# Performance work log

Measured on AMD Instinct MI355X. Metric: run time of the kernel, lower is better.

The kernel has to match this reference:

```python
import jax, jax.numpy as jnp
import numpy as np

B, L, C = 2, 8192, 256
K, NLEV = 17, 4
HALF = K // 2


def setup_inputs() -> dict:
    key = jax.random.key(0)
    ks = jax.random.split(key, 10)
    s = 0.02
    return {
        "x": jax.random.normal(ks[0], (B, L, C), jnp.float32),
        "stem_w": jax.random.normal(ks[1], (C, C, 2), jnp.float32) * s,   # Conv1d (out,in,k)
        "stem_b": jax.random.normal(ks[2], (C,), jnp.float32) * s,
        "qkv_w": jax.random.normal(ks[3], (3 * C, C), jnp.float32) * s,
        "width_w": jax.random.normal(ks[4], (1, C), jnp.float32) * s,
        "width_b": jax.random.normal(ks[5], (1,), jnp.float32) * s,
        "out_w": jax.random.normal(ks[6], (C, C), jnp.float32) * s,
        "query": jax.random.normal(ks[7], (NLEV * C,), jnp.float32) * s,
        "film_w": jax.random.normal(ks[8], (2 * C, NLEV * C), jnp.float32) * s,
        "film_b": jax.random.normal(ks[9], (2 * C,), jnp.float32) * s,
    }


def _local_attn(h, qkv_w, width_w, width_b, out_w):
    # h: (b, l, c); 1D local windowed attention with learned sigmoid distance mask
    b, l, c = h.shape
    rel_dist = jnp.abs(jnp.arange(K, dtype=h.dtype) - HALF)  # (K,)
    max_dist = float(HALF)
    scale = c ** -0.5
    qkv = h @ qkv_w.T
    q, k, v = jnp.split(qkv, 3, axis=-1)
    width = jax.nn.sigmoid(h @ width_w.T + width_b) * max_dist + 0.5  # (b,l,1)
    k_pad = jnp.pad(k, ((0, 0), (HALF, HALF), (0, 0)))
    v_pad = jnp.pad(v, ((0, 0), (HALF, HALF), (0, 0)))
    idx = jnp.arange(l)[:, None] + jnp.arange(K)[None, :]  # (l,K) indices into padded seq
    k_win = k_pad[:, idx]  # (b,l,K,c)
    v_win = v_pad[:, idx]  # (b,l,K,c)
    scores = jnp.einsum('blc,blwc->blw', q, k_win) * scale
    soft_mask = jax.nn.sigmoid((width - rel_dist) * 5.0)  # (b,l,K)
    scores = scores - (1.0 - soft_mask) * 10000.0
    attn = jax.nn.softmax(scores, axis=-1)
    o = jnp.einsum('blw,blwc->blc', attn, v_win)
    return (o + v) @ out_w.T


def _forward(x, stem_w, stem_b, qkv_w, width_w, width_b, out_w, query, film_w, film_b):
    b, l, c = x.shape
    # stem conv: Conv1d(C, C, kernel=2, padding=1), then narrow to first l positions
    h = jnp.transpose(x, (0, 2, 1))  # (B,C,L)
    h = jax.lax.conv_general_dilated(h, stem_w, (1,), [(1, 1)],
                                     dimension_numbers=('NCH', 'OIH', 'NCH'))
    h = h[:, :, :l] + stem_b[None, :, None]
    h = jnp.transpose(h, (0, 2, 1))  # (B,L,C)
    levels = []
    for i in range(NLEV):
        h = _local_attn(h, qkv_w, width_w, width_b, out_w)
        levels.append(h)
        if i < NLEV - 1:  # avg_pool(kernel=2, stride=2)
            bl = h.shape[1]
            h = h.reshape(b, bl // 2, 2, c).mean(axis=2)
    # nearest upsample each coarser level back to L (factors are exact powers of 2)
    ups = [levels[0]]
    for lvl in levels[1:]:
        ups.append(jnp.repeat(lvl, l // lvl.shape[1], axis=1))
    concat = jnp.concatenate(ups, axis=-1)  # (B,L,NLEV*C)
    gattn = jax.nn.softmax(concat @ query, axis=-1)  # (B,L)
    global_ctx = jnp.einsum('bl,bld->bd', gattn, concat)  # (B,NLEV*C)
    film = global_ctx @ film_w.T + film_b  # (B,2C)
    scale_f, bias_f = jnp.split(film, 2, axis=-1)
    return levels[0] * (1.0 + scale_f[:, None, :]) + bias_f[:, None, :]


def reference(x, stem_w, stem_b, qkv_w, width_w, width_b, out_w, query, film_w, film_b):
    return _forward(x, stem_w, stem_b, qkv_w, width_w, width_b, out_w, query, film_w, film_b)
```

## Files before the change

### kernel.cpp

```cpp
#include <hip/hip_runtime.h>
#include <math.h>

#define L_SEQ 8192
#define B_SZ  2
#define CH    256
#define NLEV  4

typedef __attribute__((ext_vector_type(8))) short bf16x8;
typedef __attribute__((ext_vector_type(4))) float f32x4;

static __device__ __forceinline__ float sigmoidf_(float x) {
    return 1.0f / (1.0f + expf(-x));
}

static __device__ __forceinline__ float bf2f_(unsigned short u) {
    union { unsigned int ui; float f; } x;
    x.ui = ((unsigned int)u) << 16;
    return x.f;
}
static __device__ __forceinline__ unsigned short f2b_(float f) {
    union { float f; unsigned int u; } x;
    x.f = f;
    unsigned int lsb = (x.u >> 16) & 1u;
    unsigned int r = x.u + 0x7fffu + lsb;
    return (unsigned short)(r >> 16);
}
static __device__ __forceinline__ float4 ldb4_(const unsigned short* p) {
    ushort4 u = *(const ushort4*)p;
    return make_float4(bf2f_(u.x), bf2f_(u.y), bf2f_(u.z), bf2f_(u.w));
}

__global__ void prep_kernel(const float* __restrict__ x,
                            const float* __restrict__ qkv_w,
                            const float* __restrict__ out_w,
                            const float* __restrict__ stem_w,
                            unsigned short* __restrict__ x16g,
                            unsigned short* __restrict__ qw16,
                            unsigned short* __restrict__ ow16,
                            unsigned short* __restrict__ sw16)
{
    int i = blockIdx.x * 256 + threadIdx.x;
    if (i < 256) { x16g[i] = 0; return; }
    i -= 256;
    if (i < 4194304) { x16g[256 + i] = f2b_(x[i]); return; }
    i -= 4194304;
    if (i < 196608) { qw16[i] = f2b_(qkv_w[i]); return; }
    i -= 196608;
    if (i < 65536) { ow16[i] = f2b_(out_w[i]); return; }
    i -= 65536;
    {
        int k = i & 511, n = i >> 9;
        float v = (k < 256) ? stem_w[(size_t)n * 512 + k * 2]
                            : stem_w[(size_t)n * 512 + (k - 256) * 2 + 1];
        sw16[i] = f2b_(v);
    }
}

__global__ __launch_bounds__(256) void stem_gemm_bf16(
    const unsigned short* __restrict__ x16g, const unsigned short* __restrict__ W,
    unsigned short* __restrict__ outB, const float* __restrict__ bias)
{
    __shared__ unsigned short As[128 * 32];
    __shared__ unsigned short Bs[128 * 32];
    const int tid  = threadIdx.x;
    const int wave = tid >> 6;
    const int lane = tid & 63;
    const int bm = blockIdx.y * 128;
    const int bn = blockIdx.x * 128;
    const int wm = (wave & 1) * 64;
    const int wn = (wave >> 1) * 64;
    const int srow = lane >> 2;
    const int scol = (lane & 3) * 8;

    f32x4 acc[4][4] = {};

    for (int k0 = 0; k0 < 512; k0 += 32) {
        __syncthreads();
        #pragma unroll
        for (int c = 0; c < 2; ++c) {
            const int chunk = c * 4 + wave;
            const int row = bm + chunk * 16 + srow;
            const int t = row & (L_SEQ - 1);
            const unsigned short* ga;
            if (k0 < 256)
                ga = x16g + (t > 0 ? (size_t)row * 256 : 0) + k0 + scol;
            else
                ga = x16g + ((size_t)row + 1) * 256 + (k0 - 256) + scol;
            const unsigned short* gw = W + (size_t)(bn + chunk * 16 + srow) * 512 + k0 + scol;
            __builtin_amdgcn_global_load_lds(
                (const __attribute__((address_space(1))) void*)ga,
                (__attribute__((address_space(3))) void*)(As + chunk * 16 * 32),
                16, 0, 0);
            __builtin_amdgcn_global_load_lds(
                (const __attribute__((address_space(1))) void*)gw,
                (__attribute__((address_space(3))) void*)(Bs + chunk * 16 * 32),
                16, 0, 0);
        }
        __syncthreads();

        bf16x8 af[4], bf[4];
        const int fr = lane & 15;
        const int kk = (lane >> 4) * 8;
        #pragma unroll
        for (int i = 0; i < 4; ++i) {
            af[i] = *(const bf16x8*)(As + (wm + i * 16 + fr) * 32 + kk);
            bf[i] = *(const bf16x8*)(Bs + (wn + i * 16 + fr) * 32 + kk);
        }
        #pragma unroll
        for (int i = 0; i < 4; ++i)
            #pragma unroll
            for (int j = 0; j < 4; ++j)
                acc[i][j] = __builtin_amdgcn_mfma_f32_16x16x32_bf16(
                    af[i], bf[j], acc[i][j], 0, 0, 0);
    }

    const int cn = lane & 15;
    const int cr = (lane >> 4) * 4;
    #pragma unroll
    for (int i = 0; i < 4; ++i)
        #pragma unroll
        for (int r = 0; r < 4; ++r) {
            const int m = bm + wm + i * 16 + cr + r;
            #pragma unroll
            for (int j = 0; j < 4; ++j) {
                const int n = bn + wn + j * 16 + cn;
                outB[(size_t)m * CH + n] = f2b_(acc[i][j][r] + bias[n]);
            }
        }
}

__global__ __launch_bounds__(256) void gemm_bf16(
    const unsigned short* __restrict__ A, const unsigned short* __restrict__ W,
    unsigned short* __restrict__ outB, int M, int N, int Kd)
{
    __shared__ unsigned short As[128 * 32];
    __shared__ unsigned short Bs[128 * 32];
    const int tid  = threadIdx.x;
    const int wave = tid >> 6;
    const int lane = tid & 63;
    const int bm = blockIdx.y * 128;
    const int bn = blockIdx.x * 128;
    const int wm = (wave & 1) * 64;
    const int wn = (wave >> 1) * 64;
    const int srow = lane >> 2;
    const int scol = (lane & 3) * 8;

    f32x4 acc[4][4] = {};

    for (int k0 = 0; k0 < Kd; k0 += 32) {
        __syncthreads();
        #pragma unroll
        for (int c = 0; c < 2; ++c) {
            const int chunk = c * 4 + wave;
            const int row = chunk * 16 + srow;
            const unsigned short* ga = A + (size_t)(bm + row) * Kd + k0 + scol;
            const unsigned short* gw = W + (size_t)(bn + row) * Kd + k0 + scol;
            __builtin_amdgcn_global_load_lds(
                (const __attribute__((address_space(1))) void*)ga,
                (__attribute__((address_space(3))) void*)(As + chunk * 16 * 32),
                16, 0, 0);
            __builtin_amdgcn_global_load_lds(
                (const __attribute__((address_space(1))) void*)gw,
                (__attribute__((address_space(3))) void*)(Bs + chunk * 16 * 32),
                16, 0, 0);
        }
        __syncthreads();

        bf16x8 af[4], bf[4];
        const int fr = lane & 15;
        const int kk = (lane >> 4) * 8;
        #pragma unroll
        for (int i = 0; i < 4; ++i) {
            af[i] = *(const bf16x8*)(As + (wm + i * 16 + fr) * 32 + kk);
            bf[i] = *(const bf16x8*)(Bs + (wn + i * 16 + fr) * 32 + kk);
        }
        #pragma unroll
        for (int i = 0; i < 4; ++i)
            #pragma unroll
            for (int j = 0; j < 4; ++j)
                acc[i][j] = __builtin_amdgcn_mfma_f32_16x16x32_bf16(
                    af[i], bf[j], acc[i][j], 0, 0, 0);
    }

    const int cn = lane & 15;
    const int cr = (lane >> 4) * 4;
    #pragma unroll
    for (int i = 0; i < 4; ++i)
        #pragma unroll
        for (int r = 0; r < 4; ++r) {
            const int m = bm + wm + i * 16 + cr + r;
            const size_t rowoff = (size_t)m * N;
            #pragma unroll
            for (int j = 0; j < 4; ++j)
                outB[rowoff + bn + wn + j * 16 + cn] = f2b_(acc[i][j][r]);
        }
}

__global__ __launch_bounds__(256) void gemm_out_bf16(
    const unsigned short* __restrict__ A, const unsigned short* __restrict__ W,
    unsigned short* __restrict__ outB, unsigned short* __restrict__ dsB, int M)
{
    __shared__ unsigned short As[128 * 32];
    __shared__ unsigned short Bs[128 * 32];
    const int tid  = threadIdx.x;
    const int wave = tid >> 6;
    const int lane = tid & 63;
    const int bm = blockIdx.y * 128;
    const int bn = blockIdx.x * 128;
    const int wm = (wave & 1) * 64;
    const int wn = (wave >> 1) * 64;
    const int srow = lane >> 2;
    const int scol = (lane & 3) * 8;

    f32x4 acc[4][4] = {};

    for (int k0 = 0; k0 < 256; k0 += 32) {
        __syncthreads();
        #pragma unroll
        for (int c = 0; c < 2; ++c) {
            const int chunk = c * 4 + wave;
            const int row = chunk * 16 + srow;
            const unsigned short* ga = A + (size_t)(bm + row) * 256 + k0 + scol;
            const unsigned short* gw = W + (size_t)(bn + row) * 256 + k0 + scol;
            __builtin_amdgcn_global_load_lds(
                (const __attribute__((address_space(1))) void*)ga,
                (__attribute__((address_space(3))) void*)(As + chunk * 16 * 32),
                16, 0, 0);
            __builtin_amdgcn_global_load_lds(
                (const __attribute__((address_space(1))) void*)gw,
                (__attribute__((address_space(3))) void*)(Bs + chunk * 16 * 32),
                16, 0, 0);
        }
        __syncthreads();

        bf16x8 af[4], bf[4];
        const int fr = lane & 15;
        const int kk = (lane >> 4) * 8;
        #pragma unroll
        for (int i = 0; i < 4; ++i) {
            af[i] = *(const bf16x8*)(As + (wm + i * 16 + fr) * 32 + kk);
            bf[i] = *(const bf16x8*)(Bs + (wn + i * 16 + fr) * 32 + kk);
        }
        #pragma unroll
        for (int i = 0; i < 4; ++i)
            #pragma unroll
            for (int j = 0; j < 4; ++j)
                acc[i][j] = __builtin_amdgcn_mfma_f32_16x16x32_bf16(
                    af[i], bf[j], acc[i][j], 0, 0, 0);
    }

    const int cn = lane & 15;
    const int cr = (lane >> 4) * 4;
    #pragma unroll
    for (int i = 0; i < 4; ++i) {
        const int base = bm + wm + i * 16 + cr;
        #pragma unroll
        for (int j = 0; j < 4; ++j) {
            const int col = bn + wn + j * 16 + cn;
            float v0 = acc[i][j][0], v1 = acc[i][j][1];
            float v2 = acc[i][j][2], v3 = acc[i][j][3];
            outB[(size_t)(base + 0) * CH + col] = f2b_(v0);
            outB[(size_t)(base + 1) * CH + col] = f2b_(v1);
            outB[(size_t)(base + 2) * CH + col] = f2b_(v2);
            outB[(size_t)(base + 3) * CH + col] = f2b_(v3);
            if (dsB) {
                dsB[(size_t)(base >> 1) * CH + col]       = f2b_(0.5f * (v0 + v1));
                dsB[(size_t)((base >> 1) + 1) * CH + col] = f2b_(0.5f * (v2 + v3));
            }
        }
    }
}

__global__ __launch_bounds__(256) void attn_mfma_kernel(
    const unsigned short* __restrict__ qkv, const unsigned short* __restrict__ h16,
    const float* __restrict__ ww, const float* __restrict__ wbp,
    unsigned short* __restrict__ ov, int l)
{
    __shared__ unsigned short kv[22528];
    __shared__ unsigned short pb[4 * 512];

    const int tid  = threadIdx.x;
    const int wave = tid >> 6;
    const int lane = tid & 63;
    const int q    = lane >> 4;
    const int n    = lane & 15;

    const int blocks_per_seq = l >> 6;
    const int b  = blockIdx.x / blocks_per_seq;
    const int t0 = (blockIdx.x % blocks_per_seq) << 6;
    const size_t seqbase = (size_t)b * l;
    const int row0 = t0 + wave * 16;

    #pragma unroll
    for (int i = 0; i < 10; ++i) {
        int task = i * 256 + tid;
        int r = task >> 5, chunk = task & 31;
        int grow = t0 - 8 + r;
        bf16x8 val = {0, 0, 0, 0, 0, 0, 0, 0};
        if (grow >= 0 && grow < l)
            val = *(const bf16x8*)(qkv + (seqbase + grow) * 768 + 256 + chunk * 8);
        *(bf16x8*)(kv + r * 272 + chunk * 8) = val;
    }

    float wdot = 0.0f;
    {
        const unsigned short* hrow = h16 + (seqbase + row0 + n) * 256 + q * 64;
        #pragma unroll
        for (int jj = 0; jj < 8; ++jj) {
            bf16x8 hv = *(const bf16x8*)(hrow + jj * 8);
            float4 wa = *((const float4*)(ww + q * 64 + jj * 8));
            float4 wc = *((const float4*)(ww + q * 64 + jj * 8 + 4));
            wdot += bf2f_(((unsigned short*)&hv)[0]) * wa.x
                  + bf2f_(((unsigned short*)&hv)[1]) * wa.y
                  + bf2f_(((unsigned short*)&hv)[2]) * wa.z
                  + bf2f_(((unsigned short*)&hv)[3]) * wa.w
                  + bf2f_(((unsigned short*)&hv)[4]) * wc.x
                  + bf2f_(((unsigned short*)&hv)[5]) * wc.y
                  + bf2f_(((unsigned short*)&hv)[6]) * wc.z
                  + bf2f_(((unsigned short*)&hv)[7]) * wc.w;
        }
    }
    wdot += __shfl_xor(wdot, 16, 64);
    wdot += __shfl_xor(wdot, 32, 64);
    const float w_n = sigmoidf_(wdot + wbp[0]) * 8.0f + 0.5f;

    __syncthreads();

    bf16x8 qf[8];
    const unsigned short* qrow = qkv + (seqbase + row0 + n) * 768;
    #pragma unroll
    for (int kk = 0; kk < 8; ++kk)
        qf[kk] = *(const bf16x8*)(qrow + kk * 32 + q * 8);

    f32x4 accS[2] = {};
    #pragma unroll
    for (int kk = 0; kk < 8; ++kk) {
        #pragma unroll
        for (int h = 0; h < 2; ++h) {
            bf16x8 bk = *(const bf16x8*)(kv + (wave * 16 + h * 16 + n) * 272 +
                                         kk * 32 + q * 8);
            accS[h] = __builtin_amdgcn_mfma_f32_16x16x32_bf16(
                qf[kk], bk, accS[h], 0, 0, 0);
        }
    }

    float wd[4];
    #pragma unroll
    for (int r = 0; r < 4; ++r) wd[r] = __shfl(w_n, q * 4 + r, 64);

    float s[2][4];
    #pragma unroll
    for (int h = 0; h < 2; ++h)
        #pragma unroll
        for (int r = 0; r < 4; ++r) {
            int ii = q * 4 + r;
            int c  = h * 16 + n;
            int w  = c - ii;
            float dist = fabsf((float)w - 8.0f);
            float sm = sigmoidf_((wd[r] - dist) * 5.0f);
            float v = accS[h][r] * 0.0625f - (1.0f - sm) * 10000.0f;
            s[h][r] = (w >= 0 && w <= 16) ? v : -3.0e38f;
        }

    float mx[4], sum[4];
    #pragma unroll
    for (int r = 0; r < 4; ++r) mx[r] = fmaxf(s[0][r], s[1][r]);
    #pragma unroll
    for (int m = 1; m < 16; m <<= 1)
        #pragma unroll
        for (int r = 0; r < 4; ++r) mx[r] = fmaxf(mx[r], __shfl_xor(mx[r], m, 64));
    float e[2][4];
    #pragma unroll
    for (int h = 0; h < 2; ++h)
        #pragma unroll
        for (int r = 0; r < 4; ++r) e[h][r] = expf(s[h][r] - mx[r]);
    #pragma unroll
    for (int r = 0; r < 4; ++r) sum[r] = e[0][r] + e[1][r];
    #pragma unroll
    for (int m = 1; m < 16; m <<= 1)
        #pragma unroll
        for (int r = 0; r < 4; ++r) sum[r] += __shfl_xor(sum[r], m, 64);

    #pragma unroll
    for (int h = 0; h < 2; ++h)
        #pragma unroll
        for (int r = 0; r < 4; ++r) {
            int ii = q * 4 + r, c = h * 16 + n;
            float p = e[h][r] / sum[r];
            if (c == ii + 8) p += 1.0f;
            pb[wave * 512 + ii * 32 + c] = f2b_(p);
        }
    __syncthreads();

    #pragma unroll
    for (int p5 = 0; p5 < 5; ++p5)
        #pragma unroll
        for (int cc = 0; cc < 2; ++cc) {
            int r = p5 * 16 + (tid & 15);
            int chunk = cc * 16 + (tid >> 4);
            int grow = t0 - 8 + r;
            bf16x8 val = {0, 0, 0, 0, 0, 0, 0, 0};
            if (grow >= 0 && grow < l)
                val = *(const bf16x8*)(qkv + (seqbase + grow) * 768 + 512 + chunk * 8);
            #pragma unroll
            for (int jj = 0; jj < 8; ++jj)
                kv[(chunk * 8 + jj) * 88 + r] = ((unsigned short*)&val)[jj];
        }
    __syncthreads();

    bf16x8 pf = *(const bf16x8*)(pb + wave * 512 + n * 32 + q * 8);
    const size_t obase = (seqbase + row0) * 256;
    #pragma unroll
    for (int chunk = 0; chunk < 16; ++chunk) {
        bf16x8 vf = *(const bf16x8*)(kv + (chunk * 16 + n) * 88 + wave * 16 + q * 8);
        f32x4 z = {};
        f32x4 o = __builtin_amdgcn_mfma_f32_16x16x32_bf16(pf, vf, z, 0, 0, 0);
        #pragma unroll
        for (int r = 0; r < 4; ++r)
            ov[obase + (size_t)(q * 4 + r) * 256 + chunk * 16 + n] = f2b_(o[r]);
    }
}

__global__ __launch_bounds__(1024) void tail_ctx_kernel(
    const unsigned short* __restrict__ l0, const unsigned short* __restrict__ l1,
    const unsigned short* __restrict__ l2, const unsigned short* __restrict__ l3,
    const float* __restrict__ query, float* __restrict__ partials,
    float* __restrict__ denomP)
{
    __shared__ float eS[128];
    const int tid = threadIdx.x;
    const int chunk = blockIdx.x, b = blockIdx.y;
    const int t0 = chunk * 128;
    const unsigned short* levp[4] = {l0, l1, l2, l3};

    const int w = tid >> 6, lane = tid & 63;
    const int lev = lane >> 4, c0 = (lane & 15) * 16;
    const unsigned short* lpbase = levp[lev] + (size_t)b * (L_SEQ >> lev) * CH;
    const float* qp = query + lev * CH + c0;
    float4 q0 = *(const float4*)(qp);
    float4 q1 = *(const float4*)(qp + 4);
    float4 q2 = *(const float4*)(qp + 8);
    float4 q3 = *(const float4*)(qp + 12);
    #pragma unroll
    for (int j = 0; j < 8; ++j) {
        int t = t0 + w * 8 + j;
        const unsigned short* p = lpbase + (size_t)(t >> lev) * CH + c0;
        float4 h0 = ldb4_(p), h1 = ldb4_(p + 4), h2 = ldb4_(p + 8), h3 = ldb4_(p + 12);
        float part = h0.x * q0.x + h0.y * q0.y + h0.z * q0.z + h0.w * q0.w
                   + h1.x * q1.x + h1.y * q1.y + h1.z * q1.z + h1.w * q1.w
                   + h2.x * q2.x + h2.y * q2.y + h2.z * q2.z + h2.w * q2.w
                   + h3.x * q3.x + h3.y * q3.y + h3.z * q3.z + h3.w * q3.w;
        #pragma unroll
        for (int m = 1; m < 64; m <<= 1) part += __shfl_xor(part, m, 64);
        if (lane == 0) eS[w * 8 + j] = expf(part);
    }
    __syncthreads();

    if (tid == 0) {
        float ds = 0.0f;
        #pragma unroll 8
        for (int i = 0; i < 128; ++i) ds += eS[i];
        denomP[b * 64 + chunk] = ds;
    }

    const int dlev = tid >> 8, c = tid & 255;
    const unsigned short* lp = levp[dlev] + (size_t)b * (L_SEQ >> dlev) * CH;
    float acc = 0.0f;
    #pragma unroll 4
    for (int t = t0; t < t0 + 128; ++t)
        acc += eS[t - t0] * bf2f_(lp[(size_t)(t >> dlev) * CH + c]);
    partials[(size_t)(b * 64 + chunk) * 1024 + tid] = acc;
}

__global__ __launch_bounds__(256) void ctx_reduce_kernel(
    const float* __restrict__ partials, const float* __restrict__ denomP,
    float* __restrict__ ctx)
{
    const int b = blockIdx.y;
    const int d = blockIdx.x * 256 + threadIdx.x;
    float acc = 0.0f;
    #pragma unroll
    for (int c = 0; c < 64; ++c) acc += partials[(size_t)(b * 64 + c) * 1024 + d];
    float den = 0.0f;
    #pragma unroll
    for (int c = 0; c < 64; ++c) den += denomP[b * 64 + c];
    ctx[b * 1024 + d] = acc / den;
}

__global__ __launch_bounds__(256) void film_kernel(
    const float* __restrict__ ctx, const float* __restrict__ fw,
    const float* __restrict__ fb, float* __restrict__ film)
{
    const int lane = threadIdx.x & 63;
    const int j = blockIdx.x * 4 + (threadIdx.x >> 6);
    float acc0 = 0.0f, acc1 = 0.0f;
    #pragma unroll
    for (int r = 0; r < 4; ++r) {
        float4 w4 = *((const float4*)(fw + (size_t)j * 1024 + r * 256) + lane);
        float4 c0 = *((const float4*)(ctx + r * 256) + lane);
        float4 c1 = *((const float4*)(ctx + 1024 + r * 256) + lane);
        acc0 += w4.x * c0.x + w4.y * c0.y + w4.z * c0.z + w4.w * c0.w;
        acc1 += w4.x * c1.x + w4.y * c1.y + w4.z * c1.z + w4.w * c1.w;
    }
    #pragma unroll
    for (int m = 1; m < 64; m <<= 1) {
        acc0 += __shfl_xor(acc0, m, 64);
        acc1 += __shfl_xor(acc1, m, 64);
    }
    if (lane == 0) {
        float b = fb[j];
        film[j] = acc0 + b;
        film[512 + j] = acc1 + b;
    }
}

__global__ void final_kernel(const unsigned short* __restrict__ lev0,
                             const float* __restrict__ film,
                             float* __restrict__ out)
{
    size_t n4 = ((size_t)blockIdx.x * 256 + threadIdx.x) * 4;
    int c = (int)(n4 & (CH - 1));
    int b = (int)(n4 >> 21);
    float4 h = ldb4_(lev0 + n4);
    const float* fs = film + b * 512;
    float4 o;
    o.x = h.x * (1.0f + fs[c + 0]) + fs[256 + c + 0];
    o.y = h.y * (1.0f + fs[c + 1]) + fs[256 + c + 1];
    o.z = h.z * (1.0f + fs[c + 2]) + fs[256 + c + 2];
    o.w = h.w * (1.0f + fs[c + 3]) + fs[256 + c + 3];
    *(float4*)(out + n4) = o;
}

extern "C" void kernel_launch(void* const* d_in, const int* in_sizes, int n_in,
                              void* d_out, int out_size, void* d_ws, size_t ws_size,
                              hipStream_t stream) {
    const float* x       = (const float*)d_in[0];
    const float* stem_w  = (const float*)d_in[1];
    const float* stem_b  = (const float*)d_in[2];
    const float* qkv_w   = (const float*)d_in[3];
    const float* width_w = (const float*)d_in[4];
    const float* width_b = (const float*)d_in[5];
    const float* out_w   = (const float*)d_in[6];
    const float* query   = (const float*)d_in[7];
    const float* film_w  = (const float*)d_in[8];
    const float* film_b  = (const float*)d_in[9];
    float* out = (float*)d_out;
    float* ws  = (float*)d_ws;

    float* partials = ws;
    float* denomP   = partials + 131072;
    float* ctx      = denomP + 128;
    float* film     = ctx + 2048;
    unsigned short* x16g  = (unsigned short*)(film + 1024);
    unsigned short* h16_0 = x16g + 4194560;
    unsigned short* h16_1 = h16_0 + 4194304;
    unsigned short* h16_2 = h16_1 + 2097152;
    unsigned short* h16_3 = h16_2 + 1048576;
    unsigned short* qkv16 = h16_3 + 524288;
    unsigned short* ov16  = qkv16 + 12582912;
    unsigned short* l16_0 = ov16 + 4194304;
    unsigned short* l16_1 = l16_0 + 4194304;
    unsigned short* l16_2 = l16_1 + 2097152;
    unsigned short* l16_3 = l16_2 + 1048576;
    unsigned short* qw16  = l16_3 + 524288;
    unsigned short* ow16  = qw16 + 196608;
    unsigned short* sw16  = ow16 + 65536;
    unsigned short* h16[4]  = {h16_0, h16_1, h16_2, h16_3};
    unsigned short* l16[4]  = {l16_0, l16_1, l16_2, l16_3};

    prep_kernel<<<(256 + 4194304 + 196608 + 65536 + 131072) / 256, 256, 0, stream>>>(
        x, qkv_w, out_w, stem_w, x16g, qw16, ow16, sw16);

    stem_gemm_bf16<<<dim3(CH / 128, B_SZ * L_SEQ / 128), 256, 0, stream>>>(
        x16g, sw16, h16_0, stem_b);

    for (int i = 0; i < NLEV; ++i) {
        const int l = L_SEQ >> i;
        const int M = B_SZ * l;
        gemm_bf16<<<dim3(768 / 128, M / 128), 256, 0, stream>>>(
            h16[i], qw16, qkv16, M, 768, CH);
        attn_mfma_kernel<<<M / 64, 256, 0, stream>>>(
            qkv16, h16[i], width_w, width_b, ov16, l);
        gemm_out_bf16<<<dim3(CH / 128, M / 128), 256, 0, stream>>>(
            ov16, ow16, l16[i], (i < NLEV - 1) ? h16[i + 1] : nullptr, M);
    }

    tail_ctx_kernel<<<dim3(64, B_SZ), 1024, 0, stream>>>(
        l16_0, l16_1, l16_2, l16_3, query, partials, denomP);
    ctx_reduce_kernel<<<dim3(4, B_SZ), 256, 0, stream>>>(partials, denomP, ctx);
    film_kernel<<<128, 256, 0, stream>>>(ctx, film_w, film_b, film);
    final_kernel<<<(B_SZ * L_SEQ * CH) / 1024, 256, 0, stream>>>(l16_0, film, out);
}
```

Before: 268.4 us.

## Fuse output projection GEMM into local attention kernel

The separate out-projection GEMM is removed and the attention kernel now stages its per-block output tile in LDS, then multiplies it by out_w in place, streaming weight tiles with global_load_lds. The fused kernel writes the level output and the avg-pooled downsample directly. This drops the ov16 round trip through global memory and one kernel launch per level. In exchange every 64-row block re-reads the whole 256x256 weight matrix, and the fused kernel holds more registers and adds extra barriers, which may cut occupancy.

```diff
diff --git a/kernel.cpp b/kernel.cpp
--- a/kernel.cpp
+++ b/kernel.cpp
@@ -196,88 +196,14 @@
         }
 }
 
-__global__ __launch_bounds__(256) void gemm_out_bf16(
-    const unsigned short* __restrict__ A, const unsigned short* __restrict__ W,
-    unsigned short* __restrict__ outB, unsigned short* __restrict__ dsB, int M)
-{
-    __shared__ unsigned short As[128 * 32];
-    __shared__ unsigned short Bs[128 * 32];
-    const int tid  = threadIdx.x;
-    const int wave = tid >> 6;
-    const int lane = tid & 63;
-    const int bm = blockIdx.y * 128;
-    const int bn = blockIdx.x * 128;
-    const int wm = (wave & 1) * 64;
-    const int wn = (wave >> 1) * 64;
-    const int srow = lane >> 2;
-    const int scol = (lane & 3) * 8;
-
-    f32x4 acc[4][4] = {};
-
-    for (int k0 = 0; k0 < 256; k0 += 32) {
-        __syncthreads();
-        #pragma unroll
-        for (int c = 0; c < 2; ++c) {
-            const int chunk = c * 4 + wave;
-            const int row = chunk * 16 + srow;
-            const unsigned short* ga = A + (size_t)(bm + row) * 256 + k0 + scol;
-            const unsigned short* gw = W + (size_t)(bn + row) * 256 + k0 + scol;
-            __builtin_amdgcn_global_load_lds(
-                (const __attribute__((address_space(1))) void*)ga,
-                (__attribute__((address_space(3))) void*)(As + chunk * 16 * 32),
-                16, 0, 0);
-            __builtin_amdgcn_global_load_lds(
-                (const __attribute__((address_space(1))) void*)gw,
-                (__attribute__((address_space(3))) void*)(Bs + chunk * 16 * 32),
-                16, 0, 0);
-        }
-        __syncthreads();
-
-        bf16x8 af[4], bf[4];
-        const int fr = lane & 15;
-        const int kk = (lane >> 4) * 8;
-        #pragma unroll
-        for (int i = 0; i < 4; ++i) {
-            af[i] = *(const bf16x8*)(As + (wm + i * 16 + fr) * 32 + kk);
-            bf[i] = *(const bf16x8*)(Bs + (wn + i * 16 + fr) * 32 + kk);
-        }
-        #pragma unroll
-        for (int i = 0; i < 4; ++i)
-            #pragma unroll
-            for (int j = 0; j < 4; ++j)
-                acc[i][j] = __builtin_amdgcn_mfma_f32_16x16x32_bf16(
-                    af[i], bf[j], acc[i][j], 0, 0, 0);
-    }
-
-    const int cn = lane & 15;
-    const int cr = (lane >> 4) * 4;
-    #pragma unroll
-    for (int i = 0; i < 4; ++i) {
-        const int base = bm + wm + i * 16 + cr;
-        #pragma unroll
-        for (int j = 0; j < 4; ++j) {
-            const int col = bn + wn + j * 16 + cn;
-            float v0 = acc[i][j][0], v1 = acc[i][j][1];
-            float v2 = acc[i][j][2], v3 = acc[i][j][3];
-            outB[(size_t)(base + 0) * CH + col] = f2b_(v0);
-            outB[(size_t)(base + 1) * CH + col] = f2b_(v1);
-            outB[(size_t)(base + 2) * CH + col] = f2b_(v2);
-            outB[(size_t)(base + 3) * CH + col] = f2b_(v3);
-            if (dsB) {
-                dsB[(size_t)(base >> 1) * CH + col]       = f2b_(0.5f * (v0 + v1));
-                dsB[(size_t)((base >> 1) + 1) * CH + col] = f2b_(0.5f * (v2 + v3));
-            }
-        }
-    }
-}
-
-__global__ __launch_bounds__(256) void attn_mfma_kernel(
+__global__ __launch_bounds__(256) void attn_out_fused(
     const unsigned short* __restrict__ qkv, const unsigned short* __restrict__ h16,
     const float* __restrict__ ww, const float* __restrict__ wbp,
-    unsigned short* __restrict__ ov, int l)
+    const unsigned short* __restrict__ ow,
+    unsigned short* __restrict__ l16out, unsigned short* __restrict__ dsB, int l)
 {
     __shared__ unsigned short kv[22528];
-    __shared__ unsigned short pb[4 * 512];
+    __shared__ unsigned short pb[2048];
 
     const int tid  = threadIdx.x;
     const int wave = tid >> 6;
@@ -409,15 +335,69 @@
     __syncthreads();
 
     bf16x8 pf = *(const bf16x8*)(pb + wave * 512 + n * 32 + q * 8);
-    const size_t obase = (seqbase + row0) * 256;
+    f32x4 o[16];
     #pragma unroll
     for (int chunk = 0; chunk < 16; ++chunk) {
         bf16x8 vf = *(const bf16x8*)(kv + (chunk * 16 + n) * 88 + wave * 16 + q * 8);
         f32x4 z = {};
-        f32x4 o = __builtin_amdgcn_mfma_f32_16x16x32_bf16(pf, vf, z, 0, 0, 0);
+        o[chunk] = __builtin_amdgcn_mfma_f32_16x16x32_bf16(pf, vf, z, 0, 0, 0);
+    }
+    __syncthreads();
+
+    unsigned short* ovS = kv;
+    unsigned short* Bs  = kv + 16640;
+
+    #pragma unroll
+    for (int chunk = 0; chunk < 16; ++chunk)
         #pragma unroll
         for (int r = 0; r < 4; ++r)
-            ov[obase + (size_t)(q * 4 + r) * 256 + chunk * 16 + n] = f2b_(o[r]);
+            ovS[(wave * 16 + q * 4 + r) * 260 + chunk * 16 + n] = f2b_(o[chunk][r]);
+    __syncthreads();
+
+    bf16x8 af2[8];
+    #pragma unroll
+    for (int kk = 0; kk < 8; ++kk)
+        af2[kk] = *(const bf16x8*)(ovS + (wave * 16 + n) * 260 + kk * 32 + q * 8);
+
+    const int base = row0 + q * 4;
+    #pragma unroll
+    for (int half = 0; half < 2; ++half) {
+        f32x4 accO[8] = {};
+        for (int k0 = 0; k0 < 8; ++k0) {
+            __syncthreads();
+            #pragma unroll
+            for (int i = 0; i < 2; ++i) {
+                int task = i * 256 + tid;
+                const unsigned short* g = ow +
+                    (size_t)(half * 128 + (task >> 2)) * 256 + k0 * 32 + (task & 3) * 8;
+                __builtin_amdgcn_global_load_lds(
+                    (const __attribute__((address_space(1))) void*)g,
+                    (__attribute__((address_space(3))) void*)(Bs + task * 8),
+                    16, 0, 0);
+            }
+            __syncthreads();
+            #pragma unroll
+            for (int j = 0; j < 8; ++j) {
+                bf16x8 bw = *(const bf16x8*)(Bs + (j * 16 + n) * 32 + q * 8);
+                accO[j] = __builtin_amdgcn_mfma_f32_16x16x32_bf16(
+                    af2[k0], bw, accO[j], 0, 0, 0);
+            }
+        }
+        #pragma unroll
+        for (int j = 0; j < 8; ++j) {
+            const int col = half * 128 + j * 16 + n;
+            float v0 = accO[j][0], v1 = accO[j][1];
+            float v2 = accO[j][2], v3 = accO[j][3];
+            l16out[(seqbase + base + 0) * CH + col] = f2b_(v0);
+            l16out[(seqbase + base + 1) * CH + col] = f2b_(v1);
+            l16out[(seqbase + base + 2) * CH + col] = f2b_(v2);
+            l16out[(seqbase + base + 3) * CH + col] = f2b_(v3);
+            if (dsB) {
+                const size_t dsrow = (seqbase + base) >> 1;
+                dsB[dsrow * CH + col]       = f2b_(0.5f * (v0 + v1));
+                dsB[(dsrow + 1) * CH + col] = f2b_(0.5f * (v2 + v3));
+            }
+        }
     }
 }
 
@@ -557,8 +537,7 @@
     unsigned short* h16_2 = h16_1 + 2097152;
     unsigned short* h16_3 = h16_2 + 1048576;
     unsigned short* qkv16 = h16_3 + 524288;
-    unsigned short* ov16  = qkv16 + 12582912;
-    unsigned short* l16_0 = ov16 + 4194304;
+    unsigned short* l16_0 = qkv16 + 12582912;
     unsigned short* l16_1 = l16_0 + 4194304;
     unsigned short* l16_2 = l16_1 + 2097152;
     unsigned short* l16_3 = l16_2 + 1048576;
@@ -579,10 +558,9 @@
         const int M = B_SZ * l;
         gemm_bf16<<<dim3(768 / 128, M / 128), 256, 0, stream>>>(
             h16[i], qw16, qkv16, M, 768, CH);
-        attn_mfma_kernel<<<M / 64, 256, 0, stream>>>(
-            qkv16, h16[i], width_w, width_b, ov16, l);
-        gemm_out_bf16<<<dim3(CH / 128, M / 128), 256, 0, stream>>>(
-            ov16, ow16, l16[i], (i < NLEV - 1) ? h16[i + 1] : nullptr, M);
+        attn_out_fused<<<M / 64, 256, 0, stream>>>(
+            qkv16, h16[i], width_w, width_b, ow16, l16[i],
+            (i < NLEV - 1) ? h16[i + 1] : nullptr, l);
     }
 
     tail_ctx_kernel<<<dim3(64, B_SZ), 1024, 0, stream>>>(
```

Result: no change. 268.9 us (+0.2%).
